# Kernel optimization log

Hardware: AMD Instinct MI355X
Metric: run time of the kernel (lower is better)

The kernel has to match this reference:

```python
import jax, jax.numpy as jnp
import numpy as np

IN, H, OUT, R, E, B = 4096, 4096, 4096, 512, 4, 64
TOT = R * IN + H * R + R * H + OUT * R  # 8388608


def setup_inputs() -> dict:
    key = jax.random.key(0)
    ks = jax.random.split(key, 7)
    s = 0.02
    x = jax.random.normal(ks[0], (B, IN), jnp.float32)
    scores = jax.random.uniform(ks[1], (E,), jnp.float32)
    delta = jax.random.normal(ks[2], (E, 1, TOT), jnp.float32) * s
    # single shared expert's base weights (all experts alias the same module)
    W1 = jax.random.normal(ks[3], (R, IN), jnp.float32) * s   # hidden_layer_u.weight
    W2 = jax.random.normal(ks[4], (H, R), jnp.float32) * s    # hidden_layer_v.weight
    W3 = jax.random.normal(ks[5], (R, H), jnp.float32) * s    # output_layer_u.weight
    W4 = jax.random.normal(ks[6], (OUT, R), jnp.float32) * s  # output_layer_v.weight
    return {"x": x, "scores": scores, "delta": delta, "W1": W1, "W2": W2, "W3": W3, "W4": W4}


def reference(x, scores, delta, W1, W2, W3, W4):
    # slice flat per-expert deltas into the four weight deltas
    d = delta[:, 0, :]                                   # [E, TOT]
    j = 0
    d1 = d[:, j:j + R * IN].reshape(E, R, IN); j += R * IN
    d2 = d[:, j:j + H * R].reshape(E, H, R);   j += H * R
    d3 = d[:, j:j + R * H].reshape(E, R, H);   j += R * H
    d4 = d[:, j:j + OUT * R].reshape(E, OUT, R)
    Wa = W1[None] + d1   # [E, R, IN]
    Wb = W2[None] + d2   # [E, H, R]
    Wc = W3[None] + d3   # [E, R, H]
    Wd = W4[None] + d4   # [E, OUT, R]
    h = jnp.einsum('bi,eri->ebr', x, Wa)                 # F.linear with W1+d1
    h = jnp.einsum('ebr,ehr->ebh', h, Wb)                # F.linear with W2+d2
    h = jax.nn.relu(h)
    h = jnp.einsum('ebh,erh->ebr', h, Wc)                # F.linear with W3+d3
    h = jnp.einsum('ebr,eor->ebo', h, Wd)                # F.linear with W4+d4
    return jnp.einsum('ebo,e->bo', h, scores)            # score-weighted sum over experts
```

## Files before the change

kernel.cpp:

```cpp
#include <hip/hip_runtime.h>
#include <hip/hip_bf16.h>

#define E_N 4
#define B_N 64
#define IN_N 4096
#define H_N 4096
#define R_N 512
#define OUT_N 4096
#define TOT_N 8388608

typedef float f32x4 __attribute__((ext_vector_type(4)));
typedef short bf16x8 __attribute__((ext_vector_type(8)));
typedef unsigned short u16x8 __attribute__((ext_vector_type(8)));

__device__ __forceinline__ unsigned short f2bf_bits(float f) {
    return __builtin_bit_cast(unsigned short, __float2bfloat16(f));
}
__device__ __forceinline__ float bfbits2f(unsigned short u) {
    return __builtin_bit_cast(float, ((unsigned)u) << 16);
}

__device__ __forceinline__ void stage16(const void* g, void* l) {
    __builtin_amdgcn_global_load_lds(
        (const __attribute__((address_space(1))) void*)g,
        (__attribute__((address_space(3))) void*)l, 16, 0, 0);
}

template<int K_TOT, int N_TOT, int KS, bool A_SHARED, bool RELU, bool OUT_BF16,
         bool CONV_A>
__global__ __launch_bounds__(256, 2)
void gemm_layer(const __hip_bfloat16* __restrict__ A, const float* __restrict__ AF,
                const float* __restrict__ W, const float* __restrict__ D,
                float* __restrict__ OutF, __hip_bfloat16* __restrict__ OutB)
{
    constexpr int KCH = K_TOT / KS;
    constexpr int NT = N_TOT / 32;
    constexpr int NTILES = KCH / 64;
    constexpr int BUFSZ = 24576;
    __shared__ __align__(16) char smem[2 * BUFSZ];

    const int bid = blockIdx.x;
    const int ks = bid % KS;
    const int nt = (bid / KS) % NT;
    const int e  = bid / (KS * NT);
    const int tid = threadIdx.x;
    const int l  = tid & 63;
    const int w  = tid >> 6;
    const int wn = w & 1;
    const int wm = w >> 1;
    const int lr = l & 15;
    const int lk = (l >> 4) << 3;

    const float* Wb = W + (size_t)(nt * 32) * K_TOT + ks * KCH;
    const float* Db = D + (size_t)e * TOT_N + (size_t)(nt * 32) * K_TOT + ks * KCH;
    const __hip_bfloat16* Ab = A + (A_SHARED ? (size_t)0 : (size_t)e * B_N * K_TOT)
                                 + ks * KCH;
    const float* AFb = AF ? (AF + (A_SHARED ? (size_t)0 : (size_t)e * B_N * K_TOT)
                                + ks * KCH)
                          : nullptr;

    const char* gsrc[6];
    int loff[6];
    int lws[6];
    int kstep[6];
    #pragma unroll
    for (int i = 0; i < 6; ++i) {
        const int q = w + i * 4;
        if (q < 8) {
            const int off = q * 1024 + l * 16;
            const int row = off >> 8;
            const int kb  = off & 255;
            gsrc[i] = (const char*)(Wb + (size_t)row * K_TOT) + (kb ^ ((row & 7) << 4));
            loff[i] = q * 1024;
            kstep[i] = 4;
        } else if (q < 16) {
            const int c = q - 8;
            const int off = c * 1024 + l * 16;
            const int row = off >> 8;
            const int kb  = off & 255;
            gsrc[i] = (const char*)(Db + (size_t)row * K_TOT) + (kb ^ ((row & 7) << 4));
            loff[i] = 8192 + c * 1024;
            kstep[i] = 4;
        } else {
            const int c = q - 16;
            const int off = c * 1024 + l * 16;
            const int row = off >> 7;
            const int kb  = off & 127;
            if (CONV_A) {
                gsrc[i] = (const char*)(AFb + (size_t)row * K_TOT) + kb * 2;
                lws[i]  = 16384 + (off & ~127) + (kb ^ ((row & 7) << 4));
                kstep[i] = 4;
            } else {
                gsrc[i] = (const char*)(Ab + (size_t)row * K_TOT) + (kb ^ ((row & 7) << 4));
                loff[i] = 16384 + c * 1024;
                kstep[i] = 2;
            }
        }
    }

    auto stage_all = [&](int kk, char* b) {
        #pragma unroll
        for (int i = 0; i < 6; ++i) {
            if (CONV_A && i >= 4) {
                const char* src = gsrc[i] + (size_t)kk * 4;
                f32x4 a0 = *(const f32x4*)(src);
                f32x4 a1 = *(const f32x4*)(src + 16);
                u16x8 o;
                #pragma unroll
                for (int j = 0; j < 4; ++j) {
                    o[j]     = f2bf_bits(a0[j]);
                    o[j + 4] = f2bf_bits(a1[j]);
                }
                *(u16x8*)(b + lws[i]) = o;
            } else {
                stage16(gsrc[i] + (size_t)kk * kstep[i], b + loff[i]);
            }
        }
    };

    f32x4 acc[2] = {};
    const int wrow = wn * 16 + lr;
    const int wswz = (wrow & 7) << 4;
    const int arow0 = wm * 32 + lr;
    const int aswz = (arow0 & 7) << 4;

    stage_all(0, smem);
    __syncthreads();

    for (int t = 0; t < NTILES; ++t) {
        if (t + 1 < NTILES)
            stage_all((t + 1) * 64, smem + ((t + 1) & 1) * BUFSZ);

        const char* buf = smem + (t & 1) * BUFSZ;
        #pragma unroll
        for (int inner = 0; inner < 2; ++inner) {
            const int b0 = (inner * 32 + lk) * 4;
            const char* wrp = buf + wrow * 256;
            const char* drp = buf + 8192 + wrow * 256;
            f32x4 w0 = *(const f32x4*)(wrp + ((b0)      ^ wswz));
            f32x4 w1 = *(const f32x4*)(wrp + ((b0 + 16) ^ wswz));
            f32x4 d0 = *(const f32x4*)(drp + ((b0)      ^ wswz));
            f32x4 d1 = *(const f32x4*)(drp + ((b0 + 16) ^ wswz));
            f32x4 s0 = w0 + d0;
            f32x4 s1 = w1 + d1;
            bf16x8 bhi, blo;
            #pragma unroll
            for (int j = 0; j < 4; ++j) {
                unsigned short h0 = f2bf_bits(s0[j]);
                bhi[j] = (short)h0;
                blo[j] = (short)f2bf_bits(s0[j] - bfbits2f(h0));
                unsigned short h1 = f2bf_bits(s1[j]);
                bhi[j + 4] = (short)h1;
                blo[j + 4] = (short)f2bf_bits(s1[j] - bfbits2f(h1));
            }
            const int ab = (inner * 32 + lk) * 2;
            #pragma unroll
            for (int mf = 0; mf < 2; ++mf) {
                const int ar = arow0 + mf * 16;
                const char* arp = buf + 16384 + ar * 128;
                bf16x8 af = *(const bf16x8*)(arp + (ab ^ aswz));
                acc[mf] = __builtin_amdgcn_mfma_f32_16x16x32_bf16(af, bhi, acc[mf], 0, 0, 0);
                acc[mf] = __builtin_amdgcn_mfma_f32_16x16x32_bf16(af, blo, acc[mf], 0, 0, 0);
            }
        }
        __syncthreads();
    }

    const int rb = (l >> 4) * 4;
    const int nrow = nt * 32 + wrow;
    #pragma unroll
    for (int j = 0; j < 2; ++j) {
        #pragma unroll
        for (int i = 0; i < 4; ++i) {
            const int row = wm * 32 + j * 16 + rb + i;
            float v = acc[j][i];
            if (RELU) v = fmaxf(v, 0.0f);
            if (OUT_BF16) {
                OutB[(size_t)e * B_N * N_TOT + (size_t)row * N_TOT + nrow] =
                    __float2bfloat16(v);
            } else {
                OutF[(size_t)(e * KS + ks) * B_N * N_TOT + (size_t)row * N_TOT + nrow] = v;
            }
        }
    }
}

template<int KS, int BN>
__global__ __launch_bounds__(256)
void reduce_ks_bf16(const float* __restrict__ P, __hip_bfloat16* __restrict__ H)
{
    const int gt = blockIdx.x * 256 + threadIdx.x;
    const int e = gt / BN;
    const int r = gt - e * BN;
    const float* base = P + (size_t)e * KS * BN + r;
    float s = 0.0f;
    #pragma unroll
    for (int k = 0; k < KS; ++k) s += base[(size_t)k * BN];
    H[gt] = __float2bfloat16(s);
}

__global__ __launch_bounds__(256)
void reduce_experts(const float* __restrict__ P, const float* __restrict__ scores,
                    float* __restrict__ out)
{
    const int gt = blockIdx.x * 256 + threadIdx.x;
    const int idx = gt * 2;
    float2 acc = {0.0f, 0.0f};
    #pragma unroll
    for (int e = 0; e < E_N; ++e) {
        const float2 v = *(const float2*)(P + (size_t)e * (B_N * OUT_N) + idx);
        const float s = scores[e];
        acc.x += s * v.x;
        acc.y += s * v.y;
    }
    *(float2*)(out + idx) = acc;
}

extern "C" void kernel_launch(void* const* d_in, const int* in_sizes, int n_in,
                              void* d_out, int out_size, void* d_ws, size_t ws_size,
                              hipStream_t stream)
{
    const float* x      = (const float*)d_in[0];
    const float* scores = (const float*)d_in[1];
    const float* delta  = (const float*)d_in[2];
    const float* W1     = (const float*)d_in[3];
    const float* W2     = (const float*)d_in[4];
    const float* W3     = (const float*)d_in[5];
    const float* W4     = (const float*)d_in[6];
    float* out = (float*)d_out;

    char* ws = (char*)d_ws;
    __hip_bfloat16* h1b = (__hip_bfloat16*)(ws + 524288);
    __hip_bfloat16* h2b = (__hip_bfloat16*)(ws + 786432);
    __hip_bfloat16* h3b = (__hip_bfloat16*)(ws + 2883584);
    float* P1 = (float*)(ws + 3145728);
    float* P3 = (float*)(ws + 7340032);
    float* P4 = (float*)(ws + 11534336);

    const float* d1 = delta;
    const float* d2 = d1 + (size_t)R_N * IN_N;
    const float* d3 = d2 + (size_t)H_N * R_N;
    const float* d4 = d3 + (size_t)R_N * H_N;

    gemm_layer<IN_N, R_N, 8, true, false, false, true>
        <<<dim3(E_N * (R_N / 32) * 8), dim3(256), 0, stream>>>(
            nullptr, x, W1, d1, P1, nullptr);
    reduce_ks_bf16<8, B_N * R_N>
        <<<dim3(E_N * B_N * R_N / 256), dim3(256), 0, stream>>>(P1, h1b);

    gemm_layer<R_N, H_N, 1, false, true, true, false>
        <<<dim3(E_N * (H_N / 32)), dim3(256), 0, stream>>>(
            h1b, nullptr, W2, d2, nullptr, h2b);

    gemm_layer<H_N, R_N, 8, false, false, false, false>
        <<<dim3(E_N * (R_N / 32) * 8), dim3(256), 0, stream>>>(
            h2b, nullptr, W3, d3, P3, nullptr);
    reduce_ks_bf16<8, B_N * R_N>
        <<<dim3(E_N * B_N * R_N / 256), dim3(256), 0, stream>>>(P3, h3b);

    gemm_layer<R_N, OUT_N, 1, false, false, false, false>
        <<<dim3(E_N * (OUT_N / 32)), dim3(256), 0, stream>>>(
            h3b, nullptr, W4, d4, P4, nullptr);

    reduce_experts<<<dim3(B_N * OUT_N / 2 / 256), dim3(256), 0, stream>>>(P4, scores, out);
}
```

Before: 48.47 us.

## Replace split-K GEMM plus reduction with in-block K-split 16x16 tile kernel

The two layers with long K (4096) used to run a split-K GEMM writing fp32 partials and then a separate reduction kernel. They now run a new kernel in which each block owns a 16x16 output tile and its four waves split K inside the block. The partial sums are combined through LDS and written straight out as bf16. This removes two kernel launches and the round trip of the partial buffers through global memory. In exchange, each block now reloads W and delta for only 16 batch rows, so four blocks per N-tile reread the same weights (4x more weight traffic, which L2 may absorb). Each block also does little MFMA work per synchronisation.

```diff
diff --git a/kernel.cpp b/kernel.cpp
--- a/kernel.cpp
+++ b/kernel.cpp
@@ -24,6 +24,141 @@
     __builtin_amdgcn_global_load_lds(
         (const __attribute__((address_space(1))) void*)g,
         (__attribute__((address_space(3))) void*)l, 16, 0, 0);
+}
+
+template<int K_TOT, bool CONV_A, bool A_SHARED>
+__global__ __launch_bounds__(256, 4)
+void gemm16(const __hip_bfloat16* __restrict__ A, const float* __restrict__ AF,
+            const float* __restrict__ W, const float* __restrict__ D,
+            __hip_bfloat16* __restrict__ OutB)
+{
+    constexpr int KK = 128;
+    constexpr int NTILES = K_TOT / KK;
+    constexpr int BUFSZ = 20480;
+    __shared__ __align__(16) char smem[2 * BUFSZ];
+
+    const int bid = blockIdx.x;
+    const int lid = (bid & 7) * 64 + (bid >> 3);
+    const int bt = lid & 3;
+    const int nt = (lid >> 2) & 31;
+    const int e  = lid >> 7;
+    const int tid = threadIdx.x;
+    const int l  = tid & 63;
+    const int w  = tid >> 6;
+
+    const char* Wb = (const char*)(W + (size_t)(nt * 16) * K_TOT);
+    const char* Db = (const char*)(D + (size_t)e * TOT_N + (size_t)(nt * 16) * K_TOT);
+    const char* Ab = CONV_A ? nullptr
+        : (const char*)(A + (A_SHARED ? (size_t)0 : (size_t)e * B_N * K_TOT)
+                          + (size_t)(bt * 16) * K_TOT);
+    const char* AFb = CONV_A
+        ? (const char*)(AF + (A_SHARED ? (size_t)0 : (size_t)e * B_N * K_TOT)
+                           + (size_t)(bt * 16) * K_TOT)
+        : nullptr;
+
+    const char* gsrc[5];
+    int loff[5], lws[5], kstep[5];
+    #pragma unroll
+    for (int i = 0; i < 5; ++i) {
+        const int q = w + i * 4;
+        if (q < 8) {
+            const int off = q * 1024 + l * 16;
+            const int row = off >> 9, kb = off & 511;
+            gsrc[i] = Wb + (size_t)row * K_TOT * 4 + (kb ^ ((row & 7) << 4));
+            loff[i] = q * 1024; kstep[i] = 512;
+        } else if (q < 16) {
+            const int c = q - 8;
+            const int off = c * 1024 + l * 16;
+            const int row = off >> 9, kb = off & 511;
+            gsrc[i] = Db + (size_t)row * K_TOT * 4 + (kb ^ ((row & 7) << 4));
+            loff[i] = 8192 + c * 1024; kstep[i] = 512;
+        } else {
+            const int c = q - 16;
+            const int off = c * 1024 + l * 16;
+            const int row = off >> 8, kb = off & 255;
+            if (CONV_A) {
+                gsrc[i] = AFb + (size_t)row * K_TOT * 4 + kb * 2;
+                lws[i]  = 16384 + (off & ~255) + (kb ^ ((row & 7) << 4));
+                kstep[i] = 512;
+            } else {
+                gsrc[i] = Ab + (size_t)row * K_TOT * 2 + (kb ^ ((row & 7) << 4));
+                loff[i] = 16384 + c * 1024; kstep[i] = 256;
+            }
+        }
+    }
+
+    auto stage_all = [&](int t, char* b) {
+        #pragma unroll
+        for (int i = 0; i < 5; ++i) {
+            const char* s = gsrc[i] + (size_t)t * kstep[i];
+            if (CONV_A && i == 4) {
+                f32x4 a0 = *(const f32x4*)(s);
+                f32x4 a1 = *(const f32x4*)(s + 16);
+                u16x8 o;
+                #pragma unroll
+                for (int j = 0; j < 4; ++j) {
+                    o[j]     = f2bf_bits(a0[j]);
+                    o[j + 4] = f2bf_bits(a1[j]);
+                }
+                *(u16x8*)(b + lws[i]) = o;
+            } else {
+                stage16(s, b + loff[i]);
+            }
+        }
+    };
+
+    const int fr  = l & 15;
+    const int kg  = l >> 4;
+    const int swz = (fr & 7) << 4;
+    const int aoff  = fr * 256 + ((w * 64 + kg * 16) ^ swz);
+    const int woffA = fr * 512 + ((w * 128 + kg * 32) ^ swz);
+    const int woffB = fr * 512 + (((w * 128 + kg * 32) + 16) ^ swz);
+
+    f32x4 acc = {};
+    stage_all(0, smem);
+    __syncthreads();
+
+    for (int t = 0; t < NTILES; ++t) {
+        if (t + 1 < NTILES)
+            stage_all(t + 1, smem + ((t + 1) & 1) * BUFSZ);
+
+        const char* buf = smem + (t & 1) * BUFSZ;
+        bf16x8 af = *(const bf16x8*)(buf + 16384 + aoff);
+        f32x4 w0 = *(const f32x4*)(buf + woffA);
+        f32x4 w1 = *(const f32x4*)(buf + woffB);
+        f32x4 d0 = *(const f32x4*)(buf + 8192 + woffA);
+        f32x4 d1 = *(const f32x4*)(buf + 8192 + woffB);
+        f32x4 s0 = w0 + d0;
+        f32x4 s1 = w1 + d1;
+        bf16x8 bhi, blo;
+        #pragma unroll
+        for (int j = 0; j < 4; ++j) {
+            unsigned short h0 = f2bf_bits(s0[j]);
+            bhi[j] = (short)h0;
+            blo[j] = (short)f2bf_bits(s0[j] - bfbits2f(h0));
+            unsigned short h1 = f2bf_bits(s1[j]);
+            bhi[j + 4] = (short)h1;
+            blo[j + 4] = (short)f2bf_bits(s1[j] - bfbits2f(h1));
+        }
+        acc = __builtin_amdgcn_mfma_f32_16x16x32_bf16(af, bhi, acc, 0, 0, 0);
+        acc = __builtin_amdgcn_mfma_f32_16x16x32_bf16(af, blo, acc, 0, 0, 0);
+        __syncthreads();
+    }
+
+    *(f32x4*)(smem + tid * 16) = acc;
+    __syncthreads();
+    if (w == 0) {
+        f32x4 s = {};
+        #pragma unroll
+        for (int wv = 0; wv < 4; ++wv)
+            s += *(const f32x4*)(smem + (wv * 64 + l) * 16);
+        #pragma unroll
+        for (int i = 0; i < 4; ++i) {
+            const int row = bt * 16 + kg * 4 + i;
+            const int col = nt * 16 + fr;
+            OutB[(size_t)e * B_N * R_N + (size_t)row * R_N + col] = __float2bfloat16(s[i]);
+        }
+    }
 }
 
 template<int K_TOT, int N_TOT, int KS, bool A_SHARED, bool RELU, bool OUT_BF16,
@@ -53,47 +188,38 @@
 
     const float* Wb = W + (size_t)(nt * 32) * K_TOT + ks * KCH;
     const float* Db = D + (size_t)e * TOT_N + (size_t)(nt * 32) * K_TOT + ks * KCH;
-    const __hip_bfloat16* Ab = A + (A_SHARED ? (size_t)0 : (size_t)e * B_N * K_TOT)
-                                 + ks * KCH;
+    const __hip_bfloat16* Ab = A ? (A + (A_SHARED ? (size_t)0 : (size_t)e * B_N * K_TOT)
+                                      + ks * KCH) : nullptr;
     const float* AFb = AF ? (AF + (A_SHARED ? (size_t)0 : (size_t)e * B_N * K_TOT)
-                                + ks * KCH)
-                          : nullptr;
+                                + ks * KCH) : nullptr;
 
     const char* gsrc[6];
-    int loff[6];
-    int lws[6];
-    int kstep[6];
+    int loff[6], lws[6], kstep[6];
     #pragma unroll
     for (int i = 0; i < 6; ++i) {
         const int q = w + i * 4;
         if (q < 8) {
             const int off = q * 1024 + l * 16;
-            const int row = off >> 8;
-            const int kb  = off & 255;
+            const int row = off >> 8, kb = off & 255;
             gsrc[i] = (const char*)(Wb + (size_t)row * K_TOT) + (kb ^ ((row & 7) << 4));
-            loff[i] = q * 1024;
-            kstep[i] = 4;
+            loff[i] = q * 1024; kstep[i] = 4;
         } else if (q < 16) {
             const int c = q - 8;
             const int off = c * 1024 + l * 16;
-            const int row = off >> 8;
-            const int kb  = off & 255;
+            const int row = off >> 8, kb = off & 255;
             gsrc[i] = (const char*)(Db + (size_t)row * K_TOT) + (kb ^ ((row & 7) << 4));
-            loff[i] = 8192 + c * 1024;
-            kstep[i] = 4;
+            loff[i] = 8192 + c * 1024; kstep[i] = 4;
         } else {
             const int c = q - 16;
             const int off = c * 1024 + l * 16;
-            const int row = off >> 7;
-            const int kb  = off & 127;
+            const int row = off >> 7, kb = off & 127;
             if (CONV_A) {
                 gsrc[i] = (const char*)(AFb + (size_t)row * K_TOT) + kb * 2;
                 lws[i]  = 16384 + (off & ~127) + (kb ^ ((row & 7) << 4));
                 kstep[i] = 4;
             } else {
                 gsrc[i] = (const char*)(Ab + (size_t)row * K_TOT) + (kb ^ ((row & 7) << 4));
-                loff[i] = 16384 + c * 1024;
-                kstep[i] = 2;
+                loff[i] = 16384 + c * 1024; kstep[i] = 2;
             }
         }
     }
@@ -175,28 +301,13 @@
             const int row = wm * 32 + j * 16 + rb + i;
             float v = acc[j][i];
             if (RELU) v = fmaxf(v, 0.0f);
-            if (OUT_BF16) {
+            if (OUT_BF16)
                 OutB[(size_t)e * B_N * N_TOT + (size_t)row * N_TOT + nrow] =
                     __float2bfloat16(v);
-            } else {
+            else
                 OutF[(size_t)(e * KS + ks) * B_N * N_TOT + (size_t)row * N_TOT + nrow] = v;
-            }
-        }
-    }
-}
-
-template<int KS, int BN>
-__global__ __launch_bounds__(256)
-void reduce_ks_bf16(const float* __restrict__ P, __hip_bfloat16* __restrict__ H)
-{
-    const int gt = blockIdx.x * 256 + threadIdx.x;
-    const int e = gt / BN;
-    const int r = gt - e * BN;
-    const float* base = P + (size_t)e * KS * BN + r;
-    float s = 0.0f;
-    #pragma unroll
-    for (int k = 0; k < KS; ++k) s += base[(size_t)k * BN];
-    H[gt] = __float2bfloat16(s);
+        }
+    }
 }
 
 __global__ __launch_bounds__(256)
@@ -233,8 +344,6 @@
     __hip_bfloat16* h1b = (__hip_bfloat16*)(ws + 524288);
     __hip_bfloat16* h2b = (__hip_bfloat16*)(ws + 786432);
     __hip_bfloat16* h3b = (__hip_bfloat16*)(ws + 2883584);
-    float* P1 = (float*)(ws + 3145728);
-    float* P3 = (float*)(ws + 7340032);
     float* P4 = (float*)(ws + 11534336);
 
     const float* d1 = delta;
@@ -242,21 +351,15 @@
     const float* d3 = d2 + (size_t)H_N * R_N;
     const float* d4 = d3 + (size_t)R_N * H_N;
 
-    gemm_layer<IN_N, R_N, 8, true, false, false, true>
-        <<<dim3(E_N * (R_N / 32) * 8), dim3(256), 0, stream>>>(
-            nullptr, x, W1, d1, P1, nullptr);
-    reduce_ks_bf16<8, B_N * R_N>
-        <<<dim3(E_N * B_N * R_N / 256), dim3(256), 0, stream>>>(P1, h1b);
+    gemm16<IN_N, true, true>
+        <<<dim3(512), dim3(256), 0, stream>>>(nullptr, x, W1, d1, h1b);
 
     gemm_layer<R_N, H_N, 1, false, true, true, false>
         <<<dim3(E_N * (H_N / 32)), dim3(256), 0, stream>>>(
             h1b, nullptr, W2, d2, nullptr, h2b);
 
-    gemm_layer<H_N, R_N, 8, false, false, false, false>
-        <<<dim3(E_N * (R_N / 32) * 8), dim3(256), 0, stream>>>(
-            h2b, nullptr, W3, d3, P3, nullptr);
-    reduce_ks_bf16<8, B_N * R_N>
-        <<<dim3(E_N * B_N * R_N / 256), dim3(256), 0, stream>>>(P3, h3b);
+    gemm16<H_N, false, false>
+        <<<dim3(512), dim3(256), 0, stream>>>(h2b, nullptr, W3, d3, h3b);
 
     gemm_layer<R_N, OUT_N, 1, false, false, false, false>
         <<<dim3(E_N * (OUT_N / 32)), dim3(256), 0, stream>>>(
```

New measurement: 66.66 us. +37.5%, slower.

## Replace split-K partial buffers and reduce kernels with atomic accumulation

Applied to the files above, without the earlier changes.

The three reduction kernels (two split-K reductions and the final expert-weighted sum) are removed. Split-K GEMMs now atomically add into fp32 buffers that are zeroed by a memset or by an earlier kernel, and the final layer atomically adds its score-weighted output directly into the result. The next layers read the fp32 activations and convert them to bf16 while staging. This cuts launches and partial-buffer traffic, but adds atomic contention and makes the summation order nondeterministic.

```diff
diff --git a/kernel.cpp b/kernel.cpp
--- a/kernel.cpp
+++ b/kernel.cpp
@@ -26,12 +26,18 @@
         (__attribute__((address_space(3))) void*)l, 16, 0, 0);
 }
 
-template<int K_TOT, int N_TOT, int KS, bool A_SHARED, bool RELU, bool OUT_BF16,
-         bool CONV_A>
+__device__ __forceinline__ void atomic_add_f32(float* p, float v) {
+    asm volatile("global_atomic_add_f32 %0, %1, off" :: "v"(p), "v"(v) : "memory");
+}
+
+template<int K_TOT, int N_TOT, int KS, bool A_SHARED, bool RELU, bool CONV_A,
+         int MODE, bool ZERO>
 __global__ __launch_bounds__(256, 2)
 void gemm_layer(const __hip_bfloat16* __restrict__ A, const float* __restrict__ AF,
                 const float* __restrict__ W, const float* __restrict__ D,
-                float* __restrict__ OutF, __hip_bfloat16* __restrict__ OutB)
+                float* __restrict__ OutF, __hip_bfloat16* __restrict__ OutB,
+                const float* __restrict__ scores, float* __restrict__ finalOut,
+                float* __restrict__ zptr, int zcount)
 {
     constexpr int KCH = K_TOT / KS;
     constexpr int NT = N_TOT / 32;
@@ -40,10 +46,16 @@
     __shared__ __align__(16) char smem[2 * BUFSZ];
 
     const int bid = blockIdx.x;
+    const int tid = threadIdx.x;
+
+    if (ZERO) {
+        for (int j = bid * 256 + tid; j < zcount; j += 512 * 256)
+            zptr[j] = 0.0f;
+    }
+
     const int ks = bid % KS;
     const int nt = (bid / KS) % NT;
     const int e  = bid / (KS * NT);
-    const int tid = threadIdx.x;
     const int l  = tid & 63;
     const int w  = tid >> 6;
     const int wn = w & 1;
@@ -53,47 +65,38 @@
 
     const float* Wb = W + (size_t)(nt * 32) * K_TOT + ks * KCH;
     const float* Db = D + (size_t)e * TOT_N + (size_t)(nt * 32) * K_TOT + ks * KCH;
-    const __hip_bfloat16* Ab = A + (A_SHARED ? (size_t)0 : (size_t)e * B_N * K_TOT)
-                                 + ks * KCH;
+    const __hip_bfloat16* Ab = A ? (A + (A_SHARED ? (size_t)0 : (size_t)e * B_N * K_TOT)
+                                      + ks * KCH) : nullptr;
     const float* AFb = AF ? (AF + (A_SHARED ? (size_t)0 : (size_t)e * B_N * K_TOT)
-                                + ks * KCH)
-                          : nullptr;
+                                + ks * KCH) : nullptr;
 
     const char* gsrc[6];
-    int loff[6];
-    int lws[6];
-    int kstep[6];
+    int loff[6], lws[6], kstep[6];
     #pragma unroll
     for (int i = 0; i < 6; ++i) {
         const int q = w + i * 4;
         if (q < 8) {
             const int off = q * 1024 + l * 16;
-            const int row = off >> 8;
-            const int kb  = off & 255;
+            const int row = off >> 8, kb = off & 255;
             gsrc[i] = (const char*)(Wb + (size_t)row * K_TOT) + (kb ^ ((row & 7) << 4));
-            loff[i] = q * 1024;
-            kstep[i] = 4;
+            loff[i] = q * 1024; kstep[i] = 4;
         } else if (q < 16) {
             const int c = q - 8;
             const int off = c * 1024 + l * 16;
-            const int row = off >> 8;
-            const int kb  = off & 255;
+            const int row = off >> 8, kb = off & 255;
             gsrc[i] = (const char*)(Db + (size_t)row * K_TOT) + (kb ^ ((row & 7) << 4));
-            loff[i] = 8192 + c * 1024;
-            kstep[i] = 4;
+            loff[i] = 8192 + c * 1024; kstep[i] = 4;
         } else {
             const int c = q - 16;
             const int off = c * 1024 + l * 16;
-            const int row = off >> 7;
-            const int kb  = off & 127;
+            const int row = off >> 7, kb = off & 127;
             if (CONV_A) {
                 gsrc[i] = (const char*)(AFb + (size_t)row * K_TOT) + kb * 2;
                 lws[i]  = 16384 + (off & ~127) + (kb ^ ((row & 7) << 4));
                 kstep[i] = 4;
             } else {
                 gsrc[i] = (const char*)(Ab + (size_t)row * K_TOT) + (kb ^ ((row & 7) << 4));
-                loff[i] = 16384 + c * 1024;
-                kstep[i] = 2;
+                loff[i] = 16384 + c * 1024; kstep[i] = 2;
             }
         }
     }
@@ -168,6 +171,7 @@
 
     const int rb = (l >> 4) * 4;
     const int nrow = nt * 32 + wrow;
+    const float se = (MODE == 3) ? scores[e] : 0.0f;
     #pragma unroll
     for (int j = 0; j < 2; ++j) {
         #pragma unroll
@@ -175,45 +179,17 @@
             const int row = wm * 32 + j * 16 + rb + i;
             float v = acc[j][i];
             if (RELU) v = fmaxf(v, 0.0f);
-            if (OUT_BF16) {
+            if (MODE == 0) {
                 OutB[(size_t)e * B_N * N_TOT + (size_t)row * N_TOT + nrow] =
                     __float2bfloat16(v);
+            } else if (MODE == 2) {
+                atomic_add_f32(OutF + (size_t)e * B_N * N_TOT
+                                    + (size_t)row * N_TOT + nrow, v);
             } else {
-                OutF[(size_t)(e * KS + ks) * B_N * N_TOT + (size_t)row * N_TOT + nrow] = v;
-            }
-        }
-    }
-}
-
-template<int KS, int BN>
-__global__ __launch_bounds__(256)
-void reduce_ks_bf16(const float* __restrict__ P, __hip_bfloat16* __restrict__ H)
-{
-    const int gt = blockIdx.x * 256 + threadIdx.x;
-    const int e = gt / BN;
-    const int r = gt - e * BN;
-    const float* base = P + (size_t)e * KS * BN + r;
-    float s = 0.0f;
-    #pragma unroll
-    for (int k = 0; k < KS; ++k) s += base[(size_t)k * BN];
-    H[gt] = __float2bfloat16(s);
-}
-
-__global__ __launch_bounds__(256)
-void reduce_experts(const float* __restrict__ P, const float* __restrict__ scores,
-                    float* __restrict__ out)
-{
-    const int gt = blockIdx.x * 256 + threadIdx.x;
-    const int idx = gt * 2;
-    float2 acc = {0.0f, 0.0f};
-    #pragma unroll
-    for (int e = 0; e < E_N; ++e) {
-        const float2 v = *(const float2*)(P + (size_t)e * (B_N * OUT_N) + idx);
-        const float s = scores[e];
-        acc.x += s * v.x;
-        acc.y += s * v.y;
-    }
-    *(float2*)(out + idx) = acc;
+                atomic_add_f32(finalOut + (size_t)row * N_TOT + nrow, se * v);
+            }
+        }
+    }
 }
 
 extern "C" void kernel_launch(void* const* d_in, const int* in_sizes, int n_in,
@@ -230,37 +206,34 @@
     float* out = (float*)d_out;
 
     char* ws = (char*)d_ws;
-    __hip_bfloat16* h1b = (__hip_bfloat16*)(ws + 524288);
-    __hip_bfloat16* h2b = (__hip_bfloat16*)(ws + 786432);
-    __hip_bfloat16* h3b = (__hip_bfloat16*)(ws + 2883584);
-    float* P1 = (float*)(ws + 3145728);
-    float* P3 = (float*)(ws + 7340032);
-    float* P4 = (float*)(ws + 11534336);
+    float* h1f = (float*)(ws);
+    float* h3f = (float*)(ws + 524288);
+    __hip_bfloat16* h2b = (__hip_bfloat16*)(ws + 1048576);
 
     const float* d1 = delta;
     const float* d2 = d1 + (size_t)R_N * IN_N;
     const float* d3 = d2 + (size_t)H_N * R_N;
     const float* d4 = d3 + (size_t)R_N * H_N;
 
-    gemm_layer<IN_N, R_N, 8, true, false, false, true>
+    hipMemsetAsync(h1f, 0, 524288, stream);
+
+    gemm_layer<IN_N, R_N, 8, true, false, true, 2, true>
         <<<dim3(E_N * (R_N / 32) * 8), dim3(256), 0, stream>>>(
-            nullptr, x, W1, d1, P1, nullptr);
-    reduce_ks_bf16<8, B_N * R_N>
-        <<<dim3(E_N * B_N * R_N / 256), dim3(256), 0, stream>>>(P1, h1b);
-
-    gemm_layer<R_N, H_N, 1, false, true, true, false>
+            nullptr, x, W1, d1, h1f, nullptr, nullptr, nullptr,
+            h3f, E_N * B_N * R_N);
+
+    gemm_layer<R_N, H_N, 1, false, true, true, 0, true>
         <<<dim3(E_N * (H_N / 32)), dim3(256), 0, stream>>>(
-            h1b, nullptr, W2, d2, nullptr, h2b);
-
-    gemm_layer<H_N, R_N, 8, false, false, false, false>
+            nullptr, h1f, W2, d2, nullptr, h2b, nullptr, nullptr,
+            out, B_N * OUT_N);
+
+    gemm_layer<H_N, R_N, 8, false, false, false, 2, false>
         <<<dim3(E_N * (R_N / 32) * 8), dim3(256), 0, stream>>>(
-            h2b, nullptr, W3, d3, P3, nullptr);
-    reduce_ks_bf16<8, B_N * R_N>
-        <<<dim3(E_N * B_N * R_N / 256), dim3(256), 0, stream>>>(P3, h3b);
-
-    gemm_layer<R_N, OUT_N, 1, false, false, false, false>
+            h2b, nullptr, W3, d3, h3f, nullptr, nullptr, nullptr,
+            nullptr, 0);
+
+    gemm_layer<R_N, OUT_N, 1, false, false, true, 3, false>
         <<<dim3(E_N * (OUT_N / 32)), dim3(256), 0, stream>>>(
-            h3b, nullptr, W4, d4, P4, nullptr);
-
-    reduce_experts<<<dim3(B_N * OUT_N / 2 / 256), dim3(256), 0, stream>>>(P4, scores, out);
-}
+            nullptr, h3f, W4, d4, nullptr, nullptr, scores, out,
+            nullptr, 0);
+}
```

New measurement: 55.92 us. +15.4%, slower.
